# Optimization experiments

Measured on AMD Instinct MI355X. Metric: run time of the kernel, lower is better.

The kernel has to match this reference:

```python
import jax, jax.numpy as jnp
import numpy as np

N, E, IN, HID, OUT = 50000, 1600000, 64, 32, 32
NEG_SLOPE = 0.2  # PyG GATConv default


def gat_conv(x, src, dst, W, a_src, a_dst, b, n):
    """Single-head PyG-style GATConv (dropout off / eval mode).
    x: [n, in], src/dst: [E+n] (self-loops already appended),
    W: [in, out], a_src/a_dst: [out], b: [out]."""
    h = x @ W                                   # [n, out]
    e_src = (h * a_src).sum(-1)                 # [n]
    e_dst = (h * a_dst).sum(-1)                 # [n]
    alpha = jax.nn.leaky_relu(e_src[src] + e_dst[dst], NEG_SLOPE)  # [Etot]
    amax = jax.ops.segment_max(alpha, dst, num_segments=n)         # per-dst max
    ex = jnp.exp(alpha - amax[dst])
    denom = jax.ops.segment_sum(ex, dst, num_segments=n)
    coef = ex / denom[dst]                      # softmax over incoming edges
    out = jax.ops.segment_sum(h[src] * coef[:, None], dst, num_segments=n)
    return out + b


def branch(x, src, dst, W1, as1, ad1, b1, W2, as2, ad2, b2, lW, lb, n):
    h = jax.nn.relu(gat_conv(x, src, dst, W1, as1, ad1, b1, n))
    h = jax.nn.relu(gat_conv(h, src, dst, W2, as2, ad2, b2, n))
    return h @ lW + lb


def setup_inputs() -> dict:
    key = jax.random.key(0)
    ks = jax.random.split(key, 32)
    inp = {
        "x": jax.random.normal(ks[0], (N, IN), dtype=jnp.float32),
        "edge_index": jax.random.randint(ks[1], (2, E), 0, N, dtype=jnp.int64),
    }
    i = 2
    for p in ("c", "r"):
        dims = [(IN, HID), (HID, HID)]
        for li, (di, do) in enumerate(dims, start=1):
            s = (2.0 / (di + do)) ** 0.5
            inp[f"{p}_W{li}"] = jax.random.normal(ks[i], (di, do), dtype=jnp.float32) * s; i += 1
            inp[f"{p}_as{li}"] = jax.random.normal(ks[i], (do,), dtype=jnp.float32) * 0.1; i += 1
            inp[f"{p}_ad{li}"] = jax.random.normal(ks[i], (do,), dtype=jnp.float32) * 0.1; i += 1
            inp[f"{p}_b{li}"] = jnp.zeros((do,), dtype=jnp.float32); i += 1
        inp[f"{p}_lW"] = jax.random.normal(ks[i], (HID, OUT), dtype=jnp.float32) * (2.0 / (HID + OUT)) ** 0.5; i += 1
        inp[f"{p}_lb"] = jnp.zeros((OUT,), dtype=jnp.float32); i += 1
    return inp


def reference(x, edge_index,
              c_W1, c_as1, c_ad1, c_b1, c_W2, c_as2, c_ad2, c_b2, c_lW, c_lb,
              r_W1, r_as1, r_ad1, r_b1, r_W2, r_as2, r_ad2, r_b2, r_lW, r_lb):
    n = x.shape[0]
    loop = jnp.arange(n, dtype=edge_index.dtype)
    src = jnp.concatenate([edge_index[0], loop])  # add_self_loops=True default
    dst = jnp.concatenate([edge_index[1], loop])
    prob_zero = jax.nn.sigmoid(branch(x, src, dst, c_W1, c_as1, c_ad1, c_b1,
                                      c_W2, c_as2, c_ad2, c_b2, c_lW, c_lb, n))
    res = branch(x, src, dst, r_W1, r_as1, r_ad1, r_b1,
                 r_W2, r_as2, r_ad2, r_b2, r_lW, r_lb, n)
    return (prob_zero, res)
```

## Files before the change

kernel.cpp:

```cpp
#include <hip/hip_runtime.h>
#include <hip/hip_fp16.h>
#include <math.h>

#define NEG_SLOPE 0.2f

#define DSHIFT 7
#define DSZ 128
#define NBUCK_MAX 512
#define PART_BLOCKS 256

typedef __attribute__((ext_vector_type(8))) _Float16 v8h;
typedef __attribute__((ext_vector_type(4))) float v4f;

__device__ __forceinline__ int ntload_i(const int* p) {
    return __builtin_nontemporal_load(p);
}

__global__ __launch_bounds__(256)
void xcast_kernel(const float* __restrict__ x, _Float16* __restrict__ xh,
                  int total4, int* __restrict__ bcount) {
    int i = blockIdx.x * blockDim.x + threadIdx.x;
    if (i < NBUCK_MAX) bcount[i] = 0;
    if (i >= total4) return;
    float4 v = ((const float4*)x)[i];
    _Float16 o[4] = {(_Float16)v.x, (_Float16)v.y, (_Float16)v.z, (_Float16)v.w};
    ((uint2*)xh)[i] = *(const uint2*)o;
}

__global__ __launch_bounds__(256)
void part_count_kernel(const int* __restrict__ ei, int E, int n, int nbuck,
                       int* __restrict__ bcount) {
    __shared__ int cnt[NBUCK_MAX];
    int t = threadIdx.x;
    for (int k = t; k < nbuck; k += 256) cnt[k] = 0;
    __syncthreads();
    int Etot = E + n;
    int chunk = (Etot + gridDim.x - 1) / gridDim.x;
    int s0 = blockIdx.x * chunk;
    int s1 = min(Etot, s0 + chunk);
    for (int i = s0 + t; i < s1; i += 256) {
        int d = (i < E) ? ntload_i(ei + E + i) : (i - E);
        if ((unsigned)d < (unsigned)n) atomicAdd(&cnt[d >> DSHIFT], 1);
    }
    __syncthreads();
    for (int k = t; k < nbuck; k += 256) {
        int c = cnt[k];
        if (c) atomicAdd(&bcount[k], c);
    }
}

__global__ void bucket_scan_kernel(const int* __restrict__ bcount,
                                   int* __restrict__ colbase,
                                   int* __restrict__ pcur,
                                   int* __restrict__ rptr,
                                   int n, int nbuck) {
    __shared__ int sm[512];
    int t = threadIdx.x;
    int v = (t < nbuck) ? bcount[t] : 0;
    sm[t] = v;
    __syncthreads();
    int x = v;
    for (int off = 1; off < 512; off <<= 1) {
        int y = (t >= off) ? sm[t - off] : 0;
        __syncthreads();
        x += y;
        sm[t] = x;
        __syncthreads();
    }
    if (t < nbuck) { colbase[t] = x - v; pcur[t] = x - v; }
    if (t == nbuck - 1) rptr[n] = x;
}

__global__ __launch_bounds__(256)
void part_write_kernel(const int* __restrict__ ei, int E, int n, int nbuck,
                       int* __restrict__ pcur,
                       unsigned* __restrict__ pairs) {
    __shared__ int cnt[NBUCK_MAX];
    __shared__ int lcur[NBUCK_MAX];
    int t = threadIdx.x;
    for (int k = t; k < nbuck; k += 256) cnt[k] = 0;
    __syncthreads();
    int Etot = E + n;
    int chunk = (Etot + gridDim.x - 1) / gridDim.x;
    int s0 = blockIdx.x * chunk;
    int s1 = min(Etot, s0 + chunk);
    for (int i = s0 + t; i < s1; i += 256) {
        int d = (i < E) ? ntload_i(ei + E + i) : (i - E);
        if ((unsigned)d < (unsigned)n) atomicAdd(&cnt[d >> DSHIFT], 1);
    }
    __syncthreads();
    for (int k = t; k < nbuck; k += 256) {
        int c = cnt[k];
        if (c) lcur[k] = atomicAdd(&pcur[k], c);
    }
    __syncthreads();
    for (int i = s0 + t; i < s1; i += 256) {
        int s, d;
        if (i < E) { s = ntload_i(ei + i); d = ntload_i(ei + E + i); }
        else       { s = d = i - E; }
        if ((unsigned)d < (unsigned)n) {
            if ((unsigned)s >= (unsigned)n) s = 0;
            int pos = atomicAdd(&lcur[d >> DSHIFT], 1);
            pairs[pos] = (unsigned)s | ((unsigned)(d & (DSZ - 1)) << 16);
        }
    }
}

__global__ __launch_bounds__(256)
void fine_kernel(const unsigned* __restrict__ pairs,
                 const int* __restrict__ colbase,
                 const int* __restrict__ bcount,
                 int* __restrict__ rptr,
                 int* __restrict__ col, int n) {
    __shared__ int cnt[DSZ];
    __shared__ int ofs[DSZ];
    int b = blockIdx.x, t = threadIdx.x;
    int p0 = colbase[b], p1 = p0 + bcount[b];
    if (t < DSZ) cnt[t] = 0;
    __syncthreads();
    for (int i = p0 + t; i < p1; i += 256)
        atomicAdd(&cnt[pairs[i] >> 16], 1);
    __syncthreads();
    int v = (t < DSZ) ? cnt[t] : 0;
    if (t < DSZ) ofs[t] = v;
    __syncthreads();
    int x = v;
    for (int off = 1; off < DSZ; off <<= 1) {
        int y = (t >= off && t < DSZ) ? ofs[t - off] : 0;
        __syncthreads();
        if (t < DSZ) { x += y; ofs[t] = x; }
        __syncthreads();
    }
    int d0 = b << DSHIFT;
    if (t < DSZ) {
        int start = p0 + x - v;
        if (d0 + t < n) rptr[d0 + t] = start;
        cnt[t] = start;
    }
    __syncthreads();
    for (int i = p0 + t; i < p1; i += 256) {
        unsigned u = pairs[i];
        int pos = atomicAdd(&cnt[u >> 16], 1);
        col[pos] = (int)(u & 0xFFFFu);
    }
}

__global__ void prep_kernel(const float* __restrict__ cW1, const float* __restrict__ rW1,
                            const float* __restrict__ cas1, const float* __restrict__ cad1,
                            const float* __restrict__ ras1, const float* __restrict__ rad1,
                            const float* __restrict__ cW2, const float* __restrict__ rW2,
                            const float* __restrict__ cas2, const float* __restrict__ cad2,
                            const float* __restrict__ ras2, const float* __restrict__ rad2,
                            const float* __restrict__ clW, const float* __restrict__ rlW,
                            _Float16* __restrict__ WB1,
                            _Float16* __restrict__ WB2,
                            _Float16* __restrict__ WBh) {
    __shared__ float f1s[2][64], f1d[2][64];
    __shared__ float f2s[2][32], f2d[2][32];
    int t = threadIdx.x;
    if (t < 128) {
        int b = t >> 6, k = t & 63;
        const float* W   = b ? rW1 : cW1;
        const float* as_ = b ? ras1 : cas1;
        const float* ad_ = b ? rad1 : cad1;
        float s1 = 0.f, s2 = 0.f;
        for (int f = 0; f < 32; ++f) {
            s1 = fmaf(W[k * 32 + f], as_[f], s1);
            s2 = fmaf(W[k * 32 + f], ad_[f], s2);
        }
        f1s[b][k] = s1;
        f1d[b][k] = s2;
    } else if (t < 192) {
        int b = (t - 128) >> 5, k = (t - 128) & 31;
        const float* W   = b ? rW2 : cW2;
        const float* as_ = b ? ras2 : cas2;
        const float* ad_ = b ? rad2 : cad2;
        float s1 = 0.f, s2 = 0.f;
        for (int f = 0; f < 32; ++f) {
            s1 = fmaf(W[k * 32 + f], as_[f], s1);
            s2 = fmaf(W[k * 32 + f], ad_[f], s2);
        }
        f2s[b][k] = s1;
        f2d[b][k] = s2;
    }
    __syncthreads();
    for (int idx = t; idx < 6144; idx += 256) {
        int blk = idx >> 9;
        int l = (idx >> 3) & 63, j = idx & 7;
        int b = blk / 6, rem = blk % 6, c = rem / 3, tt = rem % 3;
        int k = c * 32 + (l >> 4) * 8 + j;
        int nn = l & 15;
        const float* W = b ? rW1 : cW1;
        float v;
        if (tt < 2) v = W[k * 32 + tt * 16 + nn];
        else v = (nn == 0) ? f1s[b][k] : ((nn == 1) ? f1d[b][k] : 0.f);
        WB1[idx] = (_Float16)v;
    }
    for (int idx = t; idx < 3072; idx += 256) {
        int blk = idx >> 9;
        int l = (idx >> 3) & 63, j = idx & 7;
        int b = blk / 3, tt = blk % 3;
        int k = (l >> 4) * 8 + j;
        int nn = l & 15;
        const float* W = b ? rW2 : cW2;
        float v;
        if (tt < 2) v = W[k * 32 + tt * 16 + nn];
        else v = (nn == 0) ? f2s[b][k] : ((nn == 1) ? f2d[b][k] : 0.f);
        WB2[idx] = (_Float16)v;
    }
    for (int idx = t; idx < 2048; idx += 256) {
        int blk = idx >> 9;
        int l = (idx >> 3) & 63, j = idx & 7;
        int b = blk >> 1, tt = blk & 1;
        int k = (l >> 4) * 8 + j;
        int nn = l & 15;
        const float* W = b ? rlW : clW;
        WBh[idx] = (_Float16)W[k * 32 + tt * 16 + nn];
    }
}

__global__ __launch_bounds__(256)
void t1_mfma_kernel(const _Float16* __restrict__ xh,
                    const _Float16* __restrict__ WB1,
                    __half2* __restrict__ h,
                    float2* __restrict__ es2,
                    float2* __restrict__ ed2, int n) {
    int wave = (blockIdx.x * blockDim.x + threadIdx.x) >> 6;
    int lane = threadIdx.x & 63;
    int ntiles = n >> 4;
    if (wave >= ntiles) return;
    int m0 = wave << 4;
    int quad = lane >> 4, nn = lane & 15;
    const _Float16* arow = xh + (size_t)(m0 + nn) * 64 + quad * 8;
    v8h a0 = *(const v8h*)arow;
    v8h a1 = *(const v8h*)(arow + 32);
    v4f acc[2][3];
#pragma unroll
    for (int b = 0; b < 2; ++b)
#pragma unroll
        for (int tt = 0; tt < 3; ++tt) acc[b][tt] = (v4f){0.f, 0.f, 0.f, 0.f};
#pragma unroll
    for (int b = 0; b < 2; ++b) {
#pragma unroll
        for (int c = 0; c < 2; ++c) {
            v8h av = c ? a1 : a0;
#pragma unroll
            for (int tt = 0; tt < 3; ++tt) {
                v8h wb = *(const v8h*)(WB1 + (((b * 2 + c) * 3 + tt) << 9) + lane * 8);
                acc[b][tt] = __builtin_amdgcn_mfma_f32_16x16x32_f16(av, wb, acc[b][tt], 0, 0, 0);
            }
        }
    }
#pragma unroll
    for (int i = 0; i < 4; ++i) {
        int m = m0 + quad * 4 + i;
        h[(size_t)m * 32 + nn]      = __floats2half2_rn(acc[0][0][i], acc[1][0][i]);
        h[(size_t)m * 32 + 16 + nn] = __floats2half2_rn(acc[0][1][i], acc[1][1][i]);
        if (nn == 0) es2[m] = make_float2(acc[0][2][i], acc[1][2][i]);
        if (nn == 1) ed2[m] = make_float2(acc[0][2][i], acc[1][2][i]);
    }
}

__device__ __forceinline__ void load_a_frag(const __half2* __restrict__ g,
                                            int m0, int nn, int quad,
                                            v8h& aC, v8h& aR) {
    const uint4* gp = (const uint4*)(g + (size_t)(m0 + nn) * 32 + quad * 8);
    uint4 q0 = gp[0], q1 = gp[1];
    unsigned short buf[16];
    *(uint4*)buf = q0;
    *(uint4*)(buf + 8) = q1;
#pragma unroll
    for (int i = 0; i < 8; ++i) {
        ((unsigned short*)&aC)[i] = buf[2 * i];
        ((unsigned short*)&aR)[i] = buf[2 * i + 1];
    }
}

__global__ __launch_bounds__(256)
void t2_mfma_kernel(const __half2* __restrict__ g1,
                    const _Float16* __restrict__ WB2,
                    __half2* __restrict__ h2,
                    float2* __restrict__ es2o,
                    float2* __restrict__ ed2o, int n) {
    int wave = (blockIdx.x * blockDim.x + threadIdx.x) >> 6;
    int lane = threadIdx.x & 63;
    if (wave >= (n >> 4)) return;
    int m0 = wave << 4;
    int quad = lane >> 4, nn = lane & 15;
    v8h aC, aR;
    load_a_frag(g1, m0, nn, quad, aC, aR);
    v4f acc[2][3];
#pragma unroll
    for (int b = 0; b < 2; ++b)
#pragma unroll
        for (int tt = 0; tt < 3; ++tt) acc[b][tt] = (v4f){0.f, 0.f, 0.f, 0.f};
#pragma unroll
    for (int b = 0; b < 2; ++b) {
        v8h av = b ? aR : aC;
#pragma unroll
        for (int tt = 0; tt < 3; ++tt) {
            v8h wb = *(const v8h*)(WB2 + ((b * 3 + tt) << 9) + lane * 8);
            acc[b][tt] = __builtin_amdgcn_mfma_f32_16x16x32_f16(av, wb, acc[b][tt], 0, 0, 0);
        }
    }
#pragma unroll
    for (int i = 0; i < 4; ++i) {
        int m = m0 + quad * 4 + i;
        h2[(size_t)m * 32 + nn]      = __floats2half2_rn(acc[0][0][i], acc[1][0][i]);
        h2[(size_t)m * 32 + 16 + nn] = __floats2half2_rn(acc[0][1][i], acc[1][1][i]);
        if (nn == 0) es2o[m] = make_float2(acc[0][2][i], acc[1][2][i]);
        if (nn == 1) ed2o[m] = make_float2(acc[0][2][i], acc[1][2][i]);
    }
}

__global__ __launch_bounds__(256)
void head_mfma_kernel(const __half2* __restrict__ g2,
                      const _Float16* __restrict__ WBh,
                      const float* __restrict__ clb,
                      const float* __restrict__ rlb,
                      float* __restrict__ out, int n) {
    int wave = (blockIdx.x * blockDim.x + threadIdx.x) >> 6;
    int lane = threadIdx.x & 63;
    if (wave >= (n >> 4)) return;
    int m0 = wave << 4;
    int quad = lane >> 4, nn = lane & 15;
    v8h aC, aR;
    load_a_frag(g2, m0, nn, quad, aC, aR);
    v4f acc[2][2];
#pragma unroll
    for (int b = 0; b < 2; ++b)
#pragma unroll
        for (int tt = 0; tt < 2; ++tt) acc[b][tt] = (v4f){0.f, 0.f, 0.f, 0.f};
#pragma unroll
    for (int b = 0; b < 2; ++b) {
        v8h av = b ? aR : aC;
#pragma unroll
        for (int tt = 0; tt < 2; ++tt) {
            v8h wb = *(const v8h*)(WBh + ((b * 2 + tt) << 9) + lane * 8);
            acc[b][tt] = __builtin_amdgcn_mfma_f32_16x16x32_f16(av, wb, acc[b][tt], 0, 0, 0);
        }
    }
    float lb0c = clb[nn], lb1c = clb[16 + nn];
    float lb0r = rlb[nn], lb1r = rlb[16 + nn];
#pragma unroll
    for (int i = 0; i < 4; ++i) {
        int m = m0 + quad * 4 + i;
        float y0 = acc[0][0][i] + lb0c;
        float y1 = acc[0][1][i] + lb1c;
        out[(size_t)m * 32 + nn]      = 1.f / (1.f + __expf(-y0));
        out[(size_t)m * 32 + 16 + nn] = 1.f / (1.f + __expf(-y1));
        out[(size_t)n * 32 + (size_t)m * 32 + nn]      = acc[1][0][i] + lb0r;
        out[(size_t)n * 32 + (size_t)m * 32 + 16 + nn] = acc[1][1][i] + lb1r;
    }
}

__global__ __launch_bounds__(256, 8)
void agg_kernel(const int* __restrict__ rptr,
                const int* __restrict__ col,
                const __half2* __restrict__ h,
                const float2* __restrict__ es2,
                const float2* __restrict__ ed2,
                const float* __restrict__ bc,
                const float* __restrict__ br,
                __half2* __restrict__ gout, int n) {
    int grp = (blockIdx.x * blockDim.x + threadIdx.x) >> 5;
    int lane = threadIdx.x & 31;
    int sub = lane >> 2;
    int fq  = lane & 3;
    if (grp >= n) return;
    int d = grp;
    int beg = rptr[d], end = rptr[d + 1];
    float2 edv = ed2[d];
    float accC[8], accR[8];
#pragma unroll
    for (int i = 0; i < 8; ++i) { accC[i] = 0.f; accR[i] = 0.f; }
    float lc = 0.f, lr = 0.f;
    for (int base = beg; base + sub < end; base += 8) {
        int e = base + sub;
        int s = ntload_i(col + e);
        float2 ev = es2[s];
        float tc = ev.x + edv.x, tr = ev.y + edv.y;
        tc = (tc > 0.f) ? tc : NEG_SLOPE * tc;
        tr = (tr > 0.f) ? tr : NEG_SLOPE * tr;
        float exc = __expf(tc), exr = __expf(tr);
        lc += exc; lr += exr;
        const uint4* rp = (const uint4*)(h + ((size_t)s << 5));
        uint4 q0 = rp[2 * fq];
        uint4 q1 = rp[2 * fq + 1];
        const __half2* hp0 = (const __half2*)&q0;
        const __half2* hp1 = (const __half2*)&q1;
#pragma unroll
        for (int i = 0; i < 4; ++i) {
            float2 v0 = __half22float2(hp0[i]);
            float2 v1 = __half22float2(hp1[i]);
            accC[i]     = fmaf(v0.x, exc, accC[i]);
            accR[i]     = fmaf(v0.y, exr, accR[i]);
            accC[4 + i] = fmaf(v1.x, exc, accC[4 + i]);
            accR[4 + i] = fmaf(v1.y, exr, accR[4 + i]);
        }
    }
#pragma unroll
    for (int off = 4; off <= 16; off <<= 1) {
        lc += __shfl_xor(lc, off, 32);
        lr += __shfl_xor(lr, off, 32);
#pragma unroll
        for (int i = 0; i < 8; ++i) {
            accC[i] += __shfl_xor(accC[i], off, 32);
            accR[i] += __shfl_xor(accR[i], off, 32);
        }
    }
    if (sub == 0) {
        float ilc = 1.f / lc, ilr = 1.f / lr;
        __half2 o[8];
#pragma unroll
        for (int i = 0; i < 8; ++i) {
            float gc = fmaxf(accC[i] * ilc + bc[fq * 8 + i], 0.f);
            float gr = fmaxf(accR[i] * ilr + br[fq * 8 + i], 0.f);
            o[i] = __floats2half2_rn(gc, gr);
        }
        uint4* dst = (uint4*)(gout + ((size_t)d << 5) + fq * 8);
        dst[0] = *(const uint4*)&o[0];
        dst[1] = *(const uint4*)&o[4];
    }
}

extern "C" void kernel_launch(void* const* d_in, const int* in_sizes, int n_in,
                              void* d_out, int out_size, void* d_ws, size_t ws_size,
                              hipStream_t stream) {
    const float* x = (const float*)d_in[0];
    const int* ei = (const int*)d_in[1];
    const int N = in_sizes[0] / 64;
    const int E = in_sizes[1] / 2;
    const int Etot = E + N;

    const float* cW1  = (const float*)d_in[2];
    const float* cas1 = (const float*)d_in[3];
    const float* cad1 = (const float*)d_in[4];
    const float* cb1  = (const float*)d_in[5];
    const float* cW2  = (const float*)d_in[6];
    const float* cas2 = (const float*)d_in[7];
    const float* cad2 = (const float*)d_in[8];
    const float* cb2  = (const float*)d_in[9];
    const float* clW  = (const float*)d_in[10];
    const float* clb  = (const float*)d_in[11];
    const float* rW1  = (const float*)d_in[12];
    const float* ras1 = (const float*)d_in[13];
    const float* rad1 = (const float*)d_in[14];
    const float* rb1  = (const float*)d_in[15];
    const float* rW2  = (const float*)d_in[16];
    const float* ras2 = (const float*)d_in[17];
    const float* rad2 = (const float*)d_in[18];
    const float* rb2  = (const float*)d_in[19];
    const float* rlW  = (const float*)d_in[20];
    const float* rlb  = (const float*)d_in[21];

    const int nbuck = (N + DSZ - 1) >> DSHIFT;

    char* w = (char*)d_ws;
    size_t off = 0;
    auto alloc = [&](size_t bytes) {
        void* p = w + off;
        off = (off + bytes + 255) & ~(size_t)255;
        return p;
    };
    int*       rptr    = (int*)alloc((size_t)(N + 1) * 4);
    int*       bcount  = (int*)alloc(NBUCK_MAX * 4);
    int*       colbase = (int*)alloc(NBUCK_MAX * 4);
    int*       pcur    = (int*)alloc(NBUCK_MAX * 4);
    int*       col     = (int*)alloc((size_t)Etot * 4);
    unsigned*  pairs   = (unsigned*)alloc((size_t)Etot * 4);
    __half2*   h       = (__half2*)alloc((size_t)N * 32 * 4);
    __half2*   g       = (__half2*)alloc((size_t)N * 32 * 4);
    float2*    esA     = (float2*)alloc((size_t)N * 8);
    float2*    edA     = (float2*)alloc((size_t)N * 8);
    float2*    esB     = (float2*)alloc((size_t)N * 8);
    float2*    edB     = (float2*)alloc((size_t)N * 8);
    _Float16*  xh      = (_Float16*)alloc((size_t)N * 64 * 2);
    _Float16*  WB1     = (_Float16*)alloc(6144 * 2);
    _Float16*  WB2     = (_Float16*)alloc(3072 * 2);
    _Float16*  WBh     = (_Float16*)alloc(2048 * 2);
    (void)ws_size;

    float* out = (float*)d_out;
    const int node_blocks = (N * 32 + 255) / 256;
    const int xc_blocks   = (N * 64 / 4 + 255) / 256;
    const int mfma_blocks = ((N >> 4) * 64 + 255) / 256;

    xcast_kernel<<<xc_blocks, 256, 0, stream>>>(x, xh, N * 64 / 4, bcount);
    prep_kernel<<<1, 256, 0, stream>>>(cW1, rW1, cas1, cad1, ras1, rad1,
                                       cW2, rW2, cas2, cad2, ras2, rad2,
                                       clW, rlW, WB1, WB2, WBh);
    part_count_kernel<<<PART_BLOCKS, 256, 0, stream>>>(ei, E, N, nbuck, bcount);
    bucket_scan_kernel<<<1, 512, 0, stream>>>(bcount, colbase, pcur, rptr, N, nbuck);
    part_write_kernel<<<PART_BLOCKS, 256, 0, stream>>>(ei, E, N, nbuck, pcur, pairs);
    fine_kernel<<<nbuck, 256, 0, stream>>>(pairs, colbase, bcount, rptr, col, N);

    t1_mfma_kernel<<<mfma_blocks, 256, 0, stream>>>(xh, WB1, h, esA, edA, N);
    agg_kernel<<<node_blocks, 256, 0, stream>>>(
        rptr, col, h, esA, edA, cb1, rb1, g, N);

    t2_mfma_kernel<<<mfma_blocks, 256, 0, stream>>>(g, WB2, h, esB, edB, N);
    agg_kernel<<<node_blocks, 256, 0, stream>>>(
        rptr, col, h, esB, edB, cb2, rb2, g, N);
    head_mfma_kernel<<<mfma_blocks, 256, 0, stream>>>(g, WBh, clb, rlb, out, N);
}
```

Measured before the change: 278.8 us.

## Split branch features into separate fp16 arrays and aggregate each branch separately

Replaces the interleaved half2 (classifier,regressor) node feature layout with separate per-branch fp16 arrays and per-branch float attention scores. The aggregation kernel now handles one branch per launch, so it is launched twice per layer with half the accumulators and a nontemporal output store. MFMA kernels load A fragments directly without deinterleaving. This reduces register pressure and shuffle work per pass, but re-reads the CSR column index per branch and halves the useful bytes per gathered cache line.

```diff
diff --git a/kernel.cpp b/kernel.cpp
--- a/kernel.cpp
+++ b/kernel.cpp
@@ -11,6 +11,7 @@
 
 typedef __attribute__((ext_vector_type(8))) _Float16 v8h;
 typedef __attribute__((ext_vector_type(4))) float v4f;
+typedef __attribute__((ext_vector_type(4))) unsigned int v4u;
 
 __device__ __forceinline__ int ntload_i(const int* p) {
     return __builtin_nontemporal_load(p);
@@ -222,9 +223,9 @@
 __global__ __launch_bounds__(256)
 void t1_mfma_kernel(const _Float16* __restrict__ xh,
                     const _Float16* __restrict__ WB1,
-                    __half2* __restrict__ h,
-                    float2* __restrict__ es2,
-                    float2* __restrict__ ed2, int n) {
+                    _Float16* __restrict__ hC, _Float16* __restrict__ hR,
+                    float* __restrict__ esC, float* __restrict__ edC,
+                    float* __restrict__ esR, float* __restrict__ edR, int n) {
     int wave = (blockIdx.x * blockDim.x + threadIdx.x) >> 6;
     int lane = threadIdx.x & 63;
     int ntiles = n >> 4;
@@ -254,41 +255,30 @@
 #pragma unroll
     for (int i = 0; i < 4; ++i) {
         int m = m0 + quad * 4 + i;
-        h[(size_t)m * 32 + nn]      = __floats2half2_rn(acc[0][0][i], acc[1][0][i]);
-        h[(size_t)m * 32 + 16 + nn] = __floats2half2_rn(acc[0][1][i], acc[1][1][i]);
-        if (nn == 0) es2[m] = make_float2(acc[0][2][i], acc[1][2][i]);
-        if (nn == 1) ed2[m] = make_float2(acc[0][2][i], acc[1][2][i]);
-    }
-}
-
-__device__ __forceinline__ void load_a_frag(const __half2* __restrict__ g,
-                                            int m0, int nn, int quad,
-                                            v8h& aC, v8h& aR) {
-    const uint4* gp = (const uint4*)(g + (size_t)(m0 + nn) * 32 + quad * 8);
-    uint4 q0 = gp[0], q1 = gp[1];
-    unsigned short buf[16];
-    *(uint4*)buf = q0;
-    *(uint4*)(buf + 8) = q1;
-#pragma unroll
-    for (int i = 0; i < 8; ++i) {
-        ((unsigned short*)&aC)[i] = buf[2 * i];
-        ((unsigned short*)&aR)[i] = buf[2 * i + 1];
-    }
-}
-
-__global__ __launch_bounds__(256)
-void t2_mfma_kernel(const __half2* __restrict__ g1,
+        size_t r = (size_t)m * 32;
+        hC[r + nn]      = (_Float16)acc[0][0][i];
+        hC[r + 16 + nn] = (_Float16)acc[0][1][i];
+        hR[r + nn]      = (_Float16)acc[1][0][i];
+        hR[r + 16 + nn] = (_Float16)acc[1][1][i];
+        if (nn == 0) { esC[m] = acc[0][2][i]; esR[m] = acc[1][2][i]; }
+        if (nn == 1) { edC[m] = acc[0][2][i]; edR[m] = acc[1][2][i]; }
+    }
+}
+
+__global__ __launch_bounds__(256)
+void t2_mfma_kernel(const _Float16* __restrict__ gC,
+                    const _Float16* __restrict__ gR,
                     const _Float16* __restrict__ WB2,
-                    __half2* __restrict__ h2,
-                    float2* __restrict__ es2o,
-                    float2* __restrict__ ed2o, int n) {
+                    _Float16* __restrict__ hC, _Float16* __restrict__ hR,
+                    float* __restrict__ esC, float* __restrict__ edC,
+                    float* __restrict__ esR, float* __restrict__ edR, int n) {
     int wave = (blockIdx.x * blockDim.x + threadIdx.x) >> 6;
     int lane = threadIdx.x & 63;
     if (wave >= (n >> 4)) return;
     int m0 = wave << 4;
     int quad = lane >> 4, nn = lane & 15;
-    v8h aC, aR;
-    load_a_frag(g1, m0, nn, quad, aC, aR);
+    v8h aC = *(const v8h*)(gC + (size_t)(m0 + nn) * 32 + quad * 8);
+    v8h aR = *(const v8h*)(gR + (size_t)(m0 + nn) * 32 + quad * 8);
     v4f acc[2][3];
 #pragma unroll
     for (int b = 0; b < 2; ++b)
@@ -306,15 +296,19 @@
 #pragma unroll
     for (int i = 0; i < 4; ++i) {
         int m = m0 + quad * 4 + i;
-        h2[(size_t)m * 32 + nn]      = __floats2half2_rn(acc[0][0][i], acc[1][0][i]);
-        h2[(size_t)m * 32 + 16 + nn] = __floats2half2_rn(acc[0][1][i], acc[1][1][i]);
-        if (nn == 0) es2o[m] = make_float2(acc[0][2][i], acc[1][2][i]);
-        if (nn == 1) ed2o[m] = make_float2(acc[0][2][i], acc[1][2][i]);
-    }
-}
-
-__global__ __launch_bounds__(256)
-void head_mfma_kernel(const __half2* __restrict__ g2,
+        size_t r = (size_t)m * 32;
+        hC[r + nn]      = (_Float16)acc[0][0][i];
+        hC[r + 16 + nn] = (_Float16)acc[0][1][i];
+        hR[r + nn]      = (_Float16)acc[1][0][i];
+        hR[r + 16 + nn] = (_Float16)acc[1][1][i];
+        if (nn == 0) { esC[m] = acc[0][2][i]; esR[m] = acc[1][2][i]; }
+        if (nn == 1) { edC[m] = acc[0][2][i]; edR[m] = acc[1][2][i]; }
+    }
+}
+
+__global__ __launch_bounds__(256)
+void head_mfma_kernel(const _Float16* __restrict__ gC,
+                      const _Float16* __restrict__ gR,
                       const _Float16* __restrict__ WBh,
                       const float* __restrict__ clb,
                       const float* __restrict__ rlb,
@@ -324,8 +318,8 @@
     if (wave >= (n >> 4)) return;
     int m0 = wave << 4;
     int quad = lane >> 4, nn = lane & 15;
-    v8h aC, aR;
-    load_a_frag(g2, m0, nn, quad, aC, aR);
+    v8h aC = *(const v8h*)(gC + (size_t)(m0 + nn) * 32 + quad * 8);
+    v8h aR = *(const v8h*)(gR + (size_t)(m0 + nn) * 32 + quad * 8);
     v4f acc[2][2];
 #pragma unroll
     for (int b = 0; b < 2; ++b)
@@ -357,12 +351,11 @@
 __global__ __launch_bounds__(256, 8)
 void agg_kernel(const int* __restrict__ rptr,
                 const int* __restrict__ col,
-                const __half2* __restrict__ h,
-                const float2* __restrict__ es2,
-                const float2* __restrict__ ed2,
-                const float* __restrict__ bc,
-                const float* __restrict__ br,
-                __half2* __restrict__ gout, int n) {
+                const _Float16* __restrict__ hp,
+                const float* __restrict__ es,
+                const float* __restrict__ ed,
+                const float* __restrict__ bias,
+                _Float16* __restrict__ gout, int n) {
     int grp = (blockIdx.x * blockDim.x + threadIdx.x) >> 5;
     int lane = threadIdx.x & 31;
     int sub = lane >> 2;
@@ -370,57 +363,45 @@
     if (grp >= n) return;
     int d = grp;
     int beg = rptr[d], end = rptr[d + 1];
-    float2 edv = ed2[d];
-    float accC[8], accR[8];
-#pragma unroll
-    for (int i = 0; i < 8; ++i) { accC[i] = 0.f; accR[i] = 0.f; }
-    float lc = 0.f, lr = 0.f;
+    float edv = ed[d];
+    float acc[8];
+#pragma unroll
+    for (int i = 0; i < 8; ++i) acc[i] = 0.f;
+    float l = 0.f;
+#pragma unroll 2
     for (int base = beg; base + sub < end; base += 8) {
         int e = base + sub;
         int s = ntload_i(col + e);
-        float2 ev = es2[s];
-        float tc = ev.x + edv.x, tr = ev.y + edv.y;
-        tc = (tc > 0.f) ? tc : NEG_SLOPE * tc;
-        tr = (tr > 0.f) ? tr : NEG_SLOPE * tr;
-        float exc = __expf(tc), exr = __expf(tr);
-        lc += exc; lr += exr;
-        const uint4* rp = (const uint4*)(h + ((size_t)s << 5));
-        uint4 q0 = rp[2 * fq];
-        uint4 q1 = rp[2 * fq + 1];
-        const __half2* hp0 = (const __half2*)&q0;
-        const __half2* hp1 = (const __half2*)&q1;
+        float t = es[s] + edv;
+        t = (t > 0.f) ? t : NEG_SLOPE * t;
+        float ex = __expf(t);
+        l += ex;
+        uint4 q = *(const uint4*)(hp + (size_t)s * 32 + fq * 8);
+        const __half2* h2 = (const __half2*)&q;
 #pragma unroll
         for (int i = 0; i < 4; ++i) {
-            float2 v0 = __half22float2(hp0[i]);
-            float2 v1 = __half22float2(hp1[i]);
-            accC[i]     = fmaf(v0.x, exc, accC[i]);
-            accR[i]     = fmaf(v0.y, exr, accR[i]);
-            accC[4 + i] = fmaf(v1.x, exc, accC[4 + i]);
-            accR[4 + i] = fmaf(v1.y, exr, accR[4 + i]);
+            float2 v = __half22float2(h2[i]);
+            acc[2 * i]     = fmaf(v.x, ex, acc[2 * i]);
+            acc[2 * i + 1] = fmaf(v.y, ex, acc[2 * i + 1]);
         }
     }
 #pragma unroll
     for (int off = 4; off <= 16; off <<= 1) {
-        lc += __shfl_xor(lc, off, 32);
-        lr += __shfl_xor(lr, off, 32);
-#pragma unroll
-        for (int i = 0; i < 8; ++i) {
-            accC[i] += __shfl_xor(accC[i], off, 32);
-            accR[i] += __shfl_xor(accR[i], off, 32);
-        }
+        l += __shfl_xor(l, off, 32);
+#pragma unroll
+        for (int i = 0; i < 8; ++i) acc[i] += __shfl_xor(acc[i], off, 32);
     }
     if (sub == 0) {
-        float ilc = 1.f / lc, ilr = 1.f / lr;
-        __half2 o[8];
-#pragma unroll
-        for (int i = 0; i < 8; ++i) {
-            float gc = fmaxf(accC[i] * ilc + bc[fq * 8 + i], 0.f);
-            float gr = fmaxf(accR[i] * ilr + br[fq * 8 + i], 0.f);
-            o[i] = __floats2half2_rn(gc, gr);
-        }
-        uint4* dst = (uint4*)(gout + ((size_t)d << 5) + fq * 8);
-        dst[0] = *(const uint4*)&o[0];
-        dst[1] = *(const uint4*)&o[4];
+        float il = 1.f / l;
+        __half2 o[4];
+#pragma unroll
+        for (int j = 0; j < 4; ++j) {
+            float g0 = fmaxf(acc[2 * j] * il + bias[fq * 8 + 2 * j], 0.f);
+            float g1 = fmaxf(acc[2 * j + 1] * il + bias[fq * 8 + 2 * j + 1], 0.f);
+            o[j] = __floats2half2_rn(g0, g1);
+        }
+        __builtin_nontemporal_store(*(const v4u*)o,
+                                    (v4u*)(gout + (size_t)d * 32 + fq * 8));
     }
 }
 
@@ -469,12 +450,18 @@
     int*       pcur    = (int*)alloc(NBUCK_MAX * 4);
     int*       col     = (int*)alloc((size_t)Etot * 4);
     unsigned*  pairs   = (unsigned*)alloc((size_t)Etot * 4);
-    __half2*   h       = (__half2*)alloc((size_t)N * 32 * 4);
-    __half2*   g       = (__half2*)alloc((size_t)N * 32 * 4);
-    float2*    esA     = (float2*)alloc((size_t)N * 8);
-    float2*    edA     = (float2*)alloc((size_t)N * 8);
-    float2*    esB     = (float2*)alloc((size_t)N * 8);
-    float2*    edB     = (float2*)alloc((size_t)N * 8);
+    _Float16*  hC      = (_Float16*)alloc((size_t)N * 32 * 2);
+    _Float16*  hR      = (_Float16*)alloc((size_t)N * 32 * 2);
+    _Float16*  gC      = (_Float16*)alloc((size_t)N * 32 * 2);
+    _Float16*  gR      = (_Float16*)alloc((size_t)N * 32 * 2);
+    float*     esAC    = (float*)alloc((size_t)N * 4);
+    float*     edAC    = (float*)alloc((size_t)N * 4);
+    float*     esAR    = (float*)alloc((size_t)N * 4);
+    float*     edAR    = (float*)alloc((size_t)N * 4);
+    float*     esBC    = (float*)alloc((size_t)N * 4);
+    float*     edBC    = (float*)alloc((size_t)N * 4);
+    float*     esBR    = (float*)alloc((size_t)N * 4);
+    float*     edBR    = (float*)alloc((size_t)N * 4);
     _Float16*  xh      = (_Float16*)alloc((size_t)N * 64 * 2);
     _Float16*  WB1     = (_Float16*)alloc(6144 * 2);
     _Float16*  WB2     = (_Float16*)alloc(3072 * 2);
@@ -495,12 +482,18 @@
     part_write_kernel<<<PART_BLOCKS, 256, 0, stream>>>(ei, E, N, nbuck, pcur, pairs);
     fine_kernel<<<nbuck, 256, 0, stream>>>(pairs, colbase, bcount, rptr, col, N);
 
-    t1_mfma_kernel<<<mfma_blocks, 256, 0, stream>>>(xh, WB1, h, esA, edA, N);
+    t1_mfma_kernel<<<mfma_blocks, 256, 0, stream>>>(xh, WB1, hC, hR,
+                                                    esAC, edAC, esAR, edAR, N);
     agg_kernel<<<node_blocks, 256, 0, stream>>>(
-        rptr, col, h, esA, edA, cb1, rb1, g, N);
-
-    t2_mfma_kernel<<<mfma_blocks, 256, 0, stream>>>(g, WB2, h, esB, edB, N);
+        rptr, col, hC, esAC, edAC, cb1, gC, N);
     agg_kernel<<<node_blocks, 256, 0, stream>>>(
-        rptr, col, h, esB, edB, cb2, rb2, g, N);
-    head_mfma_kernel<<<mfma_blocks, 256, 0, stream>>>(g, WBh, clb, rlb, out, N);
-}
+        rptr, col, hR, esAR, edAR, rb1, gR, N);
+
+    t2_mfma_kernel<<<mfma_blocks, 256, 0, stream>>>(gC, gR, WB2, hC, hR,
+                                                    esBC, edBC, esBR, edBR, N);
+    agg_kernel<<<node_blocks, 256, 0, stream>>>(
+        rptr, col, hC, esBC, edBC, cb2, gC, N);
+    agg_kernel<<<node_blocks, 256, 0, stream>>>(
+        rptr, col, hR, esBR, edBR, rb2, gR, N);
+    head_mfma_kernel<<<mfma_blocks, 256, 0, stream>>>(gC, gR, WBh, clb, rlb, out, N);
+}
```

Result: slower. 310.5 us (+11.4%).

## Fuse x cast into layer-1 MFMA and co-launch with partition count

Applied to the files above, without the earlier changes.

Drops the separate fp32-to-fp16 cast kernel and the xh buffer: the layer-1 MFMA kernel now reads fp32 x directly and converts in registers. The partition-count work runs as extra blocks of the same launch, so the graph-bucketing count overlaps with the first feature transform. Zeroing of bcount moves into the single-block prep kernel. An unroll-by-2 pragma is added to the aggregation edge loop. These save two launches and one round trip of x through memory, at the cost of a heterogeneous kernel whose two roles may contend for resources.

```diff
diff --git a/kernel.cpp b/kernel.cpp
--- a/kernel.cpp
+++ b/kernel.cpp
@@ -16,36 +16,156 @@
     return __builtin_nontemporal_load(p);
 }
 
+__global__ void prep_kernel(const float* __restrict__ cW1, const float* __restrict__ rW1,
+                            const float* __restrict__ cas1, const float* __restrict__ cad1,
+                            const float* __restrict__ ras1, const float* __restrict__ rad1,
+                            const float* __restrict__ cW2, const float* __restrict__ rW2,
+                            const float* __restrict__ cas2, const float* __restrict__ cad2,
+                            const float* __restrict__ ras2, const float* __restrict__ rad2,
+                            const float* __restrict__ clW, const float* __restrict__ rlW,
+                            _Float16* __restrict__ WB1,
+                            _Float16* __restrict__ WB2,
+                            _Float16* __restrict__ WBh,
+                            int* __restrict__ bcount) {
+    __shared__ float f1s[2][64], f1d[2][64];
+    __shared__ float f2s[2][32], f2d[2][32];
+    int t = threadIdx.x;
+    bcount[t] = 0;
+    bcount[t + 256] = 0;
+    if (t < 128) {
+        int b = t >> 6, k = t & 63;
+        const float* W   = b ? rW1 : cW1;
+        const float* as_ = b ? ras1 : cas1;
+        const float* ad_ = b ? rad1 : cad1;
+        float s1 = 0.f, s2 = 0.f;
+        for (int f = 0; f < 32; ++f) {
+            s1 = fmaf(W[k * 32 + f], as_[f], s1);
+            s2 = fmaf(W[k * 32 + f], ad_[f], s2);
+        }
+        f1s[b][k] = s1;
+        f1d[b][k] = s2;
+    } else if (t < 192) {
+        int b = (t - 128) >> 5, k = (t - 128) & 31;
+        const float* W   = b ? rW2 : cW2;
+        const float* as_ = b ? ras2 : cas2;
+        const float* ad_ = b ? rad2 : cad2;
+        float s1 = 0.f, s2 = 0.f;
+        for (int f = 0; f < 32; ++f) {
+            s1 = fmaf(W[k * 32 + f], as_[f], s1);
+            s2 = fmaf(W[k * 32 + f], ad_[f], s2);
+        }
+        f2s[b][k] = s1;
+        f2d[b][k] = s2;
+    }
+    __syncthreads();
+    for (int idx = t; idx < 6144; idx += 256) {
+        int blk = idx >> 9;
+        int l = (idx >> 3) & 63, j = idx & 7;
+        int b = blk / 6, rem = blk % 6, c = rem / 3, tt = rem % 3;
+        int k = c * 32 + (l >> 4) * 8 + j;
+        int nn = l & 15;
+        const float* W = b ? rW1 : cW1;
+        float v;
+        if (tt < 2) v = W[k * 32 + tt * 16 + nn];
+        else v = (nn == 0) ? f1s[b][k] : ((nn == 1) ? f1d[b][k] : 0.f);
+        WB1[idx] = (_Float16)v;
+    }
+    for (int idx = t; idx < 3072; idx += 256) {
+        int blk = idx >> 9;
+        int l = (idx >> 3) & 63, j = idx & 7;
+        int b = blk / 3, tt = blk % 3;
+        int k = (l >> 4) * 8 + j;
+        int nn = l & 15;
+        const float* W = b ? rW2 : cW2;
+        float v;
+        if (tt < 2) v = W[k * 32 + tt * 16 + nn];
+        else v = (nn == 0) ? f2s[b][k] : ((nn == 1) ? f2d[b][k] : 0.f);
+        WB2[idx] = (_Float16)v;
+    }
+    for (int idx = t; idx < 2048; idx += 256) {
+        int blk = idx >> 9;
+        int l = (idx >> 3) & 63, j = idx & 7;
+        int b = blk >> 1, tt = blk & 1;
+        int k = (l >> 4) * 8 + j;
+        int nn = l & 15;
+        const float* W = b ? rlW : clW;
+        WBh[idx] = (_Float16)W[k * 32 + tt * 16 + nn];
+    }
+}
+
 __global__ __launch_bounds__(256)
-void xcast_kernel(const float* __restrict__ x, _Float16* __restrict__ xh,
-                  int total4, int* __restrict__ bcount) {
-    int i = blockIdx.x * blockDim.x + threadIdx.x;
-    if (i < NBUCK_MAX) bcount[i] = 0;
-    if (i >= total4) return;
-    float4 v = ((const float4*)x)[i];
-    _Float16 o[4] = {(_Float16)v.x, (_Float16)v.y, (_Float16)v.z, (_Float16)v.w};
-    ((uint2*)xh)[i] = *(const uint2*)o;
-}
-
-__global__ __launch_bounds__(256)
-void part_count_kernel(const int* __restrict__ ei, int E, int n, int nbuck,
-                       int* __restrict__ bcount) {
+void t1pc_kernel(const float* __restrict__ x,
+                 const _Float16* __restrict__ WB1,
+                 __half2* __restrict__ h,
+                 float2* __restrict__ es2,
+                 float2* __restrict__ ed2, int n,
+                 const int* __restrict__ ei, int E, int nbuck,
+                 int* __restrict__ bcount, int t1b) {
     __shared__ int cnt[NBUCK_MAX];
-    int t = threadIdx.x;
-    for (int k = t; k < nbuck; k += 256) cnt[k] = 0;
-    __syncthreads();
-    int Etot = E + n;
-    int chunk = (Etot + gridDim.x - 1) / gridDim.x;
-    int s0 = blockIdx.x * chunk;
-    int s1 = min(Etot, s0 + chunk);
-    for (int i = s0 + t; i < s1; i += 256) {
-        int d = (i < E) ? ntload_i(ei + E + i) : (i - E);
-        if ((unsigned)d < (unsigned)n) atomicAdd(&cnt[d >> DSHIFT], 1);
-    }
-    __syncthreads();
-    for (int k = t; k < nbuck; k += 256) {
-        int c = cnt[k];
-        if (c) atomicAdd(&bcount[k], c);
+    if ((int)blockIdx.x >= t1b) {
+        int b = blockIdx.x - t1b;
+        int t = threadIdx.x;
+        for (int k = t; k < nbuck; k += 256) cnt[k] = 0;
+        __syncthreads();
+        int Etot = E + n;
+        int chunk = (Etot + PART_BLOCKS - 1) / PART_BLOCKS;
+        int s0 = b * chunk;
+        int s1 = min(Etot, s0 + chunk);
+        for (int i = s0 + t; i < s1; i += 256) {
+            int d = (i < E) ? ntload_i(ei + E + i) : (i - E);
+            if ((unsigned)d < (unsigned)n) atomicAdd(&cnt[d >> DSHIFT], 1);
+        }
+        __syncthreads();
+        for (int k = t; k < nbuck; k += 256) {
+            int c = cnt[k];
+            if (c) atomicAdd(&bcount[k], c);
+        }
+        return;
+    }
+    int wave = (blockIdx.x * blockDim.x + threadIdx.x) >> 6;
+    int lane = threadIdx.x & 63;
+    int ntiles = n >> 4;
+    if (wave >= ntiles) return;
+    int m0 = wave << 4;
+    int quad = lane >> 4, nn = lane & 15;
+    const float* xrow = x + (size_t)(m0 + nn) * 64 + quad * 8;
+    float4 f0 = *(const float4*)xrow;
+    float4 f1 = *(const float4*)(xrow + 4);
+    float4 f2 = *(const float4*)(xrow + 32);
+    float4 f3 = *(const float4*)(xrow + 36);
+    v8h a0, a1;
+    a0[0] = (_Float16)f0.x; a0[1] = (_Float16)f0.y;
+    a0[2] = (_Float16)f0.z; a0[3] = (_Float16)f0.w;
+    a0[4] = (_Float16)f1.x; a0[5] = (_Float16)f1.y;
+    a0[6] = (_Float16)f1.z; a0[7] = (_Float16)f1.w;
+    a1[0] = (_Float16)f2.x; a1[1] = (_Float16)f2.y;
+    a1[2] = (_Float16)f2.z; a1[3] = (_Float16)f2.w;
+    a1[4] = (_Float16)f3.x; a1[5] = (_Float16)f3.y;
+    a1[6] = (_Float16)f3.z; a1[7] = (_Float16)f3.w;
+    v4f acc[2][3];
+#pragma unroll
+    for (int b = 0; b < 2; ++b)
+#pragma unroll
+        for (int tt = 0; tt < 3; ++tt) acc[b][tt] = (v4f){0.f, 0.f, 0.f, 0.f};
+#pragma unroll
+    for (int b = 0; b < 2; ++b) {
+#pragma unroll
+        for (int c = 0; c < 2; ++c) {
+            v8h av = c ? a1 : a0;
+#pragma unroll
+            for (int tt = 0; tt < 3; ++tt) {
+                v8h wb = *(const v8h*)(WB1 + (((b * 2 + c) * 3 + tt) << 9) + lane * 8);
+                acc[b][tt] = __builtin_amdgcn_mfma_f32_16x16x32_f16(av, wb, acc[b][tt], 0, 0, 0);
+            }
+        }
+    }
+#pragma unroll
+    for (int i = 0; i < 4; ++i) {
+        int m = m0 + quad * 4 + i;
+        h[(size_t)m * 32 + nn]      = __floats2half2_rn(acc[0][0][i], acc[1][0][i]);
+        h[(size_t)m * 32 + 16 + nn] = __floats2half2_rn(acc[0][1][i], acc[1][1][i]);
+        if (nn == 0) es2[m] = make_float2(acc[0][2][i], acc[1][2][i]);
+        if (nn == 1) ed2[m] = make_float2(acc[0][2][i], acc[1][2][i]);
     }
 }
 
@@ -142,122 +262,6 @@
         unsigned u = pairs[i];
         int pos = atomicAdd(&cnt[u >> 16], 1);
         col[pos] = (int)(u & 0xFFFFu);
-    }
-}
-
-__global__ void prep_kernel(const float* __restrict__ cW1, const float* __restrict__ rW1,
-                            const float* __restrict__ cas1, const float* __restrict__ cad1,
-                            const float* __restrict__ ras1, const float* __restrict__ rad1,
-                            const float* __restrict__ cW2, const float* __restrict__ rW2,
-                            const float* __restrict__ cas2, const float* __restrict__ cad2,
-                            const float* __restrict__ ras2, const float* __restrict__ rad2,
-                            const float* __restrict__ clW, const float* __restrict__ rlW,
-                            _Float16* __restrict__ WB1,
-                            _Float16* __restrict__ WB2,
-                            _Float16* __restrict__ WBh) {
-    __shared__ float f1s[2][64], f1d[2][64];
-    __shared__ float f2s[2][32], f2d[2][32];
-    int t = threadIdx.x;
-    if (t < 128) {
-        int b = t >> 6, k = t & 63;
-        const float* W   = b ? rW1 : cW1;
-        const float* as_ = b ? ras1 : cas1;
-        const float* ad_ = b ? rad1 : cad1;
-        float s1 = 0.f, s2 = 0.f;
-        for (int f = 0; f < 32; ++f) {
-            s1 = fmaf(W[k * 32 + f], as_[f], s1);
-            s2 = fmaf(W[k * 32 + f], ad_[f], s2);
-        }
-        f1s[b][k] = s1;
-        f1d[b][k] = s2;
-    } else if (t < 192) {
-        int b = (t - 128) >> 5, k = (t - 128) & 31;
-        const float* W   = b ? rW2 : cW2;
-        const float* as_ = b ? ras2 : cas2;
-        const float* ad_ = b ? rad2 : cad2;
-        float s1 = 0.f, s2 = 0.f;
-        for (int f = 0; f < 32; ++f) {
-            s1 = fmaf(W[k * 32 + f], as_[f], s1);
-            s2 = fmaf(W[k * 32 + f], ad_[f], s2);
-        }
-        f2s[b][k] = s1;
-        f2d[b][k] = s2;
-    }
-    __syncthreads();
-    for (int idx = t; idx < 6144; idx += 256) {
-        int blk = idx >> 9;
-        int l = (idx >> 3) & 63, j = idx & 7;
-        int b = blk / 6, rem = blk % 6, c = rem / 3, tt = rem % 3;
-        int k = c * 32 + (l >> 4) * 8 + j;
-        int nn = l & 15;
-        const float* W = b ? rW1 : cW1;
-        float v;
-        if (tt < 2) v = W[k * 32 + tt * 16 + nn];
-        else v = (nn == 0) ? f1s[b][k] : ((nn == 1) ? f1d[b][k] : 0.f);
-        WB1[idx] = (_Float16)v;
-    }
-    for (int idx = t; idx < 3072; idx += 256) {
-        int blk = idx >> 9;
-        int l = (idx >> 3) & 63, j = idx & 7;
-        int b = blk / 3, tt = blk % 3;
-        int k = (l >> 4) * 8 + j;
-        int nn = l & 15;
-        const float* W = b ? rW2 : cW2;
-        float v;
-        if (tt < 2) v = W[k * 32 + tt * 16 + nn];
-        else v = (nn == 0) ? f2s[b][k] : ((nn == 1) ? f2d[b][k] : 0.f);
-        WB2[idx] = (_Float16)v;
-    }
-    for (int idx = t; idx < 2048; idx += 256) {
-        int blk = idx >> 9;
-        int l = (idx >> 3) & 63, j = idx & 7;
-        int b = blk >> 1, tt = blk & 1;
-        int k = (l >> 4) * 8 + j;
-        int nn = l & 15;
-        const float* W = b ? rlW : clW;
-        WBh[idx] = (_Float16)W[k * 32 + tt * 16 + nn];
-    }
-}
-
-__global__ __launch_bounds__(256)
-void t1_mfma_kernel(const _Float16* __restrict__ xh,
-                    const _Float16* __restrict__ WB1,
-                    __half2* __restrict__ h,
-                    float2* __restrict__ es2,
-                    float2* __restrict__ ed2, int n) {
-    int wave = (blockIdx.x * blockDim.x + threadIdx.x) >> 6;
-    int lane = threadIdx.x & 63;
-    int ntiles = n >> 4;
-    if (wave >= ntiles) return;
-    int m0 = wave << 4;
-    int quad = lane >> 4, nn = lane & 15;
-    const _Float16* arow = xh + (size_t)(m0 + nn) * 64 + quad * 8;
-    v8h a0 = *(const v8h*)arow;
-    v8h a1 = *(const v8h*)(arow + 32);
-    v4f acc[2][3];
-#pragma unroll
-    for (int b = 0; b < 2; ++b)
-#pragma unroll
-        for (int tt = 0; tt < 3; ++tt) acc[b][tt] = (v4f){0.f, 0.f, 0.f, 0.f};
-#pragma unroll
-    for (int b = 0; b < 2; ++b) {
-#pragma unroll
-        for (int c = 0; c < 2; ++c) {
-            v8h av = c ? a1 : a0;
-#pragma unroll
-            for (int tt = 0; tt < 3; ++tt) {
-                v8h wb = *(const v8h*)(WB1 + (((b * 2 + c) * 3 + tt) << 9) + lane * 8);
-                acc[b][tt] = __builtin_amdgcn_mfma_f32_16x16x32_f16(av, wb, acc[b][tt], 0, 0, 0);
-            }
-        }
-    }
-#pragma unroll
-    for (int i = 0; i < 4; ++i) {
-        int m = m0 + quad * 4 + i;
-        h[(size_t)m * 32 + nn]      = __floats2half2_rn(acc[0][0][i], acc[1][0][i]);
-        h[(size_t)m * 32 + 16 + nn] = __floats2half2_rn(acc[0][1][i], acc[1][1][i]);
-        if (nn == 0) es2[m] = make_float2(acc[0][2][i], acc[1][2][i]);
-        if (nn == 1) ed2[m] = make_float2(acc[0][2][i], acc[1][2][i]);
     }
 }
 
@@ -375,6 +379,7 @@
 #pragma unroll
     for (int i = 0; i < 8; ++i) { accC[i] = 0.f; accR[i] = 0.f; }
     float lc = 0.f, lr = 0.f;
+#pragma unroll 2
     for (int base = beg; base + sub < end; base += 8) {
         int e = base + sub;
         int s = ntload_i(col + e);
@@ -475,7 +480,6 @@
     float2*    edA     = (float2*)alloc((size_t)N * 8);
     float2*    esB     = (float2*)alloc((size_t)N * 8);
     float2*    edB     = (float2*)alloc((size_t)N * 8);
-    _Float16*  xh      = (_Float16*)alloc((size_t)N * 64 * 2);
     _Float16*  WB1     = (_Float16*)alloc(6144 * 2);
     _Float16*  WB2     = (_Float16*)alloc(3072 * 2);
     _Float16*  WBh     = (_Float16*)alloc(2048 * 2);
@@ -483,19 +487,17 @@
 
     float* out = (float*)d_out;
     const int node_blocks = (N * 32 + 255) / 256;
-    const int xc_blocks   = (N * 64 / 4 + 255) / 256;
     const int mfma_blocks = ((N >> 4) * 64 + 255) / 256;
 
-    xcast_kernel<<<xc_blocks, 256, 0, stream>>>(x, xh, N * 64 / 4, bcount);
     prep_kernel<<<1, 256, 0, stream>>>(cW1, rW1, cas1, cad1, ras1, rad1,
                                        cW2, rW2, cas2, cad2, ras2, rad2,
-                                       clW, rlW, WB1, WB2, WBh);
-    part_count_kernel<<<PART_BLOCKS, 256, 0, stream>>>(ei, E, N, nbuck, bcount);
+                                       clW, rlW, WB1, WB2, WBh, bcount);
+    t1pc_kernel<<<mfma_blocks + PART_BLOCKS, 256, 0, stream>>>(
+        x, WB1, h, esA, edA, N, ei, E, nbuck, bcount, mfma_blocks);
     bucket_scan_kernel<<<1, 512, 0, stream>>>(bcount, colbase, pcur, rptr, N, nbuck);
     part_write_kernel<<<PART_BLOCKS, 256, 0, stream>>>(ei, E, N, nbuck, pcur, pairs);
     fine_kernel<<<nbuck, 256, 0, stream>>>(pairs, colbase, bcount, rptr, col, N);
 
-    t1_mfma_kernel<<<mfma_blocks, 256, 0, stream>>>(xh, WB1, h, esA, edA, N);
     agg_kernel<<<node_blocks, 256, 0, stream>>>(
         rptr, col, h, esA, edA, cb1, rb1, g, N);
 
```

New measurement: 278.4 us. No clear change (-0.1%).
